# Performance work log

Hardware: AMD Instinct MI355X
Metric: run time of the kernel (lower is better)

The kernel has to match this reference:

```python
import jax, jax.numpy as jnp
import numpy as np

B, LI, LC, H = 16, 2048, 2048, 1024


def setup_inputs() -> dict:
    key = jax.random.key(0)
    k1, k2, k3, k4 = jax.random.split(key, 4)
    inp = jax.random.normal(k1, (B, LI, H), dtype=jnp.float32)
    ctx = jax.random.normal(k2, (B, LC, H), dtype=jnp.float32)
    # mask out the last quarter of context positions (True = masked), never a full row
    context_mask = jnp.broadcast_to(jnp.arange(LC) >= (3 * LC) // 4, (B, LC))
    W = jax.random.normal(k3, (H, H), dtype=jnp.float32) * (1.0 / np.sqrt(H))
    b = jax.random.normal(k4, (H,), dtype=jnp.float32) * 0.01
    return {"input": inp, "context": ctx, "context_mask": context_mask, "W": W, "b": b}


def reference(input, context, context_mask, W, b):
    # shared relu-projected linear for query and key/value sides
    q = jax.nn.relu(jnp.einsum('bih,oh->bio', input, W) + b)    # [B, Li, H]
    k = jax.nn.relu(jnp.einsum('bjh,oh->bjo', context, W) + b)  # [B, Lc, H]
    scores = jnp.einsum('bid,bjd->bij', q, k)                    # [B, Li, Lc], no scaling
    scores = jnp.where(context_mask[:, None, :], -jnp.inf, scores)
    probs = jax.nn.softmax(scores, axis=2)
    return jnp.einsum('bij,bjd->bid', probs, k)                  # weighted sum of context hiddens
```

## Files before the change

kernel.cpp:

```cpp
#include <hip/hip_runtime.h>

typedef _Float16 half8 __attribute__((ext_vector_type(8)));
typedef _Float16 half4 __attribute__((ext_vector_type(4)));
typedef float floatx4 __attribute__((ext_vector_type(4)));

#define OFF_X    0L
#define OFF_S    0L
#define OFF_P    67108864L
#define OFF_W    134217728L
#define OFF_QK   136314880L
#define OFF_KT   270532608L
#define OFF_MASK 337641472L
#define WS_NEED  337674240L

__device__ __forceinline__ void glds16(const void* g, void* l) {
  __builtin_amdgcn_global_load_lds(
      (__attribute__((address_space(1))) void*)(void*)(g),
      (__attribute__((address_space(3))) void*)(l), 16, 0, 0);
}

__global__ void mask_canon(const unsigned* __restrict__ raw,
                           unsigned char* __restrict__ outm) {
  __shared__ int flag;
  int t = threadIdx.x;
  if (t == 0) flag = 0;
  __syncthreads();
  int loc = 0;
  for (int i = t; i < 8192; i += 256)
    if (raw[i] > 1u) loc = 1;
  if (loc) flag = 1;
  __syncthreads();
  if (flag) {
    const unsigned char* b8 = (const unsigned char*)raw;
    for (int j = t; j < 32768; j += 256) outm[j] = (b8[j] != 0);
  } else {
    const int* r32 = (const int*)raw;
    for (int j = t; j < 32768; j += 256) outm[j] = (r32[j] != 0);
  }
}

__global__ __launch_bounds__(256) void cvt_f32_f16(const float* __restrict__ x,
                                                   _Float16* __restrict__ y, long n) {
  long i = ((long)blockIdx.x * 256 + threadIdx.x) * 4;
  if (i + 3 < n) {
    float4 v = *(const float4*)(x + i);
    half4 h;
    h[0] = (_Float16)v.x; h[1] = (_Float16)v.y;
    h[2] = (_Float16)v.z; h[3] = (_Float16)v.w;
    *(half4*)(y + i) = h;
  }
}

template <bool EPI>
__global__ __launch_bounds__(512, 2)
void gemm_nt3(const _Float16* __restrict__ A, long sAz,
              const _Float16* __restrict__ B, long sBz,
              void* __restrict__ Cv, long sCz,
              const float* __restrict__ bias, int K, int ldc) {
  __shared__ _Float16 lds[81920];
  const int t = threadIdx.x;
  const int l = t & 63;
  const int w = t >> 6;
  const int wr = w >> 2, wc = w & 3;
  const int l15 = l & 15, quad = l >> 4;
  const int srow = l >> 3;
  const int gchunk = (l & 7) ^ (srow & 7);
  const int sbase = w * 8;

  const _Float16* Ag = A + (long)blockIdx.z * sAz + (long)blockIdx.y * 256 * (long)K;
  const _Float16* Bg = B + (long)blockIdx.z * sBz + (long)blockIdx.x * 256 * (long)K;

  _Float16* const As = lds;
  _Float16* const Bs = lds + 32768;

  const int arow = wr * 128 + l15;
  const int brow = wc * 64 + l15;
  const int ccA = (quad ^ (arow & 7)) << 3;
  const int ccB = (quad ^ (brow & 7)) << 3;

  floatx4 acc[8][4] = {};
  const int NT = K >> 6;

#define STG(gp, dst, rnd, kt)                                                  \
  glds16(gp + (long)((rnd) * 64 + sbase + srow) * K + (kt) + gchunk * 8,       \
         (dst) + ((rnd) * 64 + sbase) * 64)
#define MM(mh)                                                                 \
  do {                                                                         \
    _Pragma("unroll") for (int mi_ = 0; mi_ < 4; ++mi_)                        \
      _Pragma("unroll") for (int ni_ = 0; ni_ < 4; ++ni_)                      \
        acc[(mh) * 4 + mi_][ni_] = __builtin_amdgcn_mfma_f32_16x16x32_f16(     \
            af[mi_], bf[ni_], acc[(mh) * 4 + mi_][ni_], 0, 0, 0);              \
  } while (0)
#define PH_HEAD()                                                              \
  __builtin_amdgcn_s_barrier();                                                \
  asm volatile("s_waitcnt lgkmcnt(0)" ::: "memory");                           \
  __builtin_amdgcn_s_setprio(1)
#define PH_TAIL()                                                              \
  __builtin_amdgcn_s_setprio(0)

  STG(Ag, As, 0, 0); STG(Ag, As, 1, 0); STG(Ag, As, 2, 0); STG(Ag, As, 3, 0);
  STG(Bg, Bs, 0, 0); STG(Bg, Bs, 1, 0); STG(Bg, Bs, 2, 0); STG(Bg, Bs, 3, 0);
  {
    const int k1 = (NT > 1 ? 64 : 0);
    _Float16* b1 = Bs + 16384;
    STG(Bg, b1, 0, k1); STG(Bg, b1, 1, k1); STG(Bg, b1, 2, k1); STG(Bg, b1, 3, k1);
  }
  asm volatile("s_waitcnt vmcnt(4)" ::: "memory");
  __builtin_amdgcn_s_barrier();

  int bq = 0, bq2 = 2;
  for (int tt = 0; tt < NT; ++tt) {
    const _Float16* Ap = As + (tt & 1) * 16384;
    const _Float16* Bp = Bs + bq * 16384;
    _Float16* Anx = As + ((tt + 1) & 1) * 16384;
    _Float16* Bnx = Bs + bq2 * 16384;
    const int kt1 = ((tt + 1 < NT) ? tt + 1 : NT - 1) << 6;
    const int kt2 = ((tt + 2 < NT) ? tt + 2 : NT - 1) << 6;
    half8 af[4], bf[4];

#pragma unroll
    for (int ni = 0; ni < 4; ++ni) bf[ni] = *(const half8*)(Bp + (brow + ni * 16) * 64 + ccB);
#pragma unroll
    for (int mi = 0; mi < 4; ++mi) af[mi] = *(const half8*)(Ap + (arow + mi * 16) * 64 + ccA);
    STG(Ag, Anx, 0, kt1);
    STG(Ag, Anx, 1, kt1);
    PH_HEAD();
    MM(0);
    PH_TAIL();
    __builtin_amdgcn_s_barrier();

#pragma unroll
    for (int mi = 0; mi < 4; ++mi)
      af[mi] = *(const half8*)(Ap + (arow + (mi + 4) * 16) * 64 + ccA);
    STG(Ag, Anx, 2, kt1);
    STG(Ag, Anx, 3, kt1);
    PH_HEAD();
    MM(1);
    PH_TAIL();
    __builtin_amdgcn_s_barrier();

#pragma unroll
    for (int ni = 0; ni < 4; ++ni)
      bf[ni] = *(const half8*)(Bp + (brow + ni * 16) * 64 + (ccB ^ 32));
#pragma unroll
    for (int mi = 0; mi < 4; ++mi)
      af[mi] = *(const half8*)(Ap + (arow + mi * 16) * 64 + (ccA ^ 32));
    STG(Bg, Bnx, 0, kt2);
    STG(Bg, Bnx, 1, kt2);
    PH_HEAD();
    MM(0);
    PH_TAIL();
    __builtin_amdgcn_s_barrier();

#pragma unroll
    for (int mi = 0; mi < 4; ++mi)
      af[mi] = *(const half8*)(Ap + (arow + (mi + 4) * 16) * 64 + (ccA ^ 32));
    STG(Bg, Bnx, 2, kt2);
    STG(Bg, Bnx, 3, kt2);
    PH_HEAD();
    MM(1);
    PH_TAIL();
    asm volatile("s_waitcnt vmcnt(4)" ::: "memory");
    __builtin_amdgcn_s_barrier();

    bq = (bq == 2) ? 0 : bq + 1;
    bq2 = (bq2 == 2) ? 0 : bq2 + 1;
  }
  asm volatile("s_waitcnt vmcnt(0)" ::: "memory");
  __syncthreads();
#undef STG
#undef MM
#undef PH_HEAD
#undef PH_TAIL

  const long cbase = (long)blockIdx.z * sCz + (long)blockIdx.y * 256 * (long)ldc +
                     (long)blockIdx.x * 256;
  const int rowb = quad * 4;
  if constexpr (EPI) {
    float bv[4];
#pragma unroll
    for (int ni = 0; ni < 4; ++ni) bv[ni] = bias[blockIdx.x * 256 + wc * 64 + ni * 16 + l15];
#pragma unroll
    for (int mi = 0; mi < 8; ++mi)
#pragma unroll
      for (int ni = 0; ni < 4; ++ni) {
        const int col = wc * 64 + ni * 16 + l15;
#pragma unroll
        for (int p = 0; p < 4; ++p) {
          const int row = wr * 128 + mi * 16 + rowb + p;
          lds[row * 264 + (((col >> 3) ^ (row & 7)) << 3) + (col & 7)] =
              (_Float16)fmaxf(acc[mi][ni][p] + bv[ni], 0.f);
        }
      }
    __syncthreads();
    _Float16* Cp = (_Float16*)Cv + cbase;
#pragma unroll
    for (int pp = 0; pp < 16; ++pp) {
      const int r = (t >> 5) + 16 * pp;
      const int c = t & 31;
      half8 v = *(const half8*)(lds + r * 264 + ((c ^ (r & 7)) << 3));
      *(half8*)(Cp + (long)r * ldc + c * 8) = v;
    }
  } else {
    float* Cp = (float*)Cv + cbase;
#pragma unroll
    for (int mi = 0; mi < 8; ++mi)
#pragma unroll
      for (int ni = 0; ni < 4; ++ni) {
        const int col = wc * 64 + ni * 16 + l15;
#pragma unroll
        for (int p = 0; p < 4; ++p) {
          const int row = wr * 128 + mi * 16 + rowb + p;
          Cp[(long)row * ldc + col] = acc[mi][ni][p];
        }
      }
  }
}

__global__ __launch_bounds__(256) void transpose_k(const _Float16* __restrict__ Km,
                                                   _Float16* __restrict__ KT) {
  __shared__ _Float16 tile[64 * 72];
  const int t = threadIdx.x;
  const long b = blockIdx.z;
  const _Float16* src = Km + (b * 2048 + blockIdx.x * 64) * 1024 + blockIdx.y * 64;
  {
    const int jl = t >> 2, hc = (t & 3) * 16;
    half8 v0 = *(const half8*)(src + (long)jl * 1024 + hc);
    half8 v1 = *(const half8*)(src + (long)jl * 1024 + hc + 8);
    *(half8*)&tile[jl * 72 + hc] = v0;
    *(half8*)&tile[jl * 72 + hc + 8] = v1;
  }
  __syncthreads();
  {
    const int hl = t >> 2, jc = (t & 3) * 16;
    half8 o0, o1;
#pragma unroll
    for (int jj = 0; jj < 8; jj++) o0[jj] = tile[(jc + jj) * 72 + hl];
#pragma unroll
    for (int jj = 0; jj < 8; jj++) o1[jj] = tile[(jc + 8 + jj) * 72 + hl];
    long off = (b * 1024 + blockIdx.y * 64 + hl) * 2048 + blockIdx.x * 64 + jc;
    *(half8*)(KT + off) = o0;
    *(half8*)(KT + off + 8) = o1;
  }
}

__global__ __launch_bounds__(256) void softmax_k(const float* __restrict__ S,
                                                 _Float16* __restrict__ P,
                                                 const unsigned char* __restrict__ mask,
                                                 int b0) {
  const int i = blockIdx.x, z = blockIdx.y, t = threadIdx.x;
  const float* s = S + ((long)z * 2048 + i) * 2048;
  const unsigned char* mrow = mask + (long)(b0 + z) * 2048;
  const int base0 = t * 4, base1 = 1024 + t * 4;
  float4 a0 = *(const float4*)(s + base0);
  float4 a1 = *(const float4*)(s + base1);
  float v[8] = {a0.x, a0.y, a0.z, a0.w, a1.x, a1.y, a1.z, a1.w};
  const float NINF = -__builtin_inff();
#pragma unroll
  for (int k = 0; k < 4; k++) {
    if (mrow[base0 + k]) v[k] = NINF;
    if (mrow[base1 + k]) v[4 + k] = NINF;
  }
  float mx = v[0];
#pragma unroll
  for (int k = 1; k < 8; k++) mx = fmaxf(mx, v[k]);
#pragma unroll
  for (int o = 32; o >= 1; o >>= 1) mx = fmaxf(mx, __shfl_xor(mx, o, 64));
  __shared__ float redm[4], reds[4];
  if ((t & 63) == 0) redm[t >> 6] = mx;
  __syncthreads();
  mx = fmaxf(fmaxf(redm[0], redm[1]), fmaxf(redm[2], redm[3]));
  float e[8], sm = 0.f;
#pragma unroll
  for (int k = 0; k < 8; k++) { e[k] = __expf(v[k] - mx); sm += e[k]; }
#pragma unroll
  for (int o = 32; o >= 1; o >>= 1) sm += __shfl_xor(sm, o, 64);
  if ((t & 63) == 0) reds[t >> 6] = sm;
  __syncthreads();
  sm = reds[0] + reds[1] + reds[2] + reds[3];
  const float inv = 1.0f / sm;
  _Float16* p = P + ((long)z * 2048 + i) * 2048;
  half4 h0, h1;
#pragma unroll
  for (int k = 0; k < 4; k++) { h0[k] = (_Float16)(e[k] * inv); h1[k] = (_Float16)(e[4 + k] * inv); }
  *(half4*)(p + base0) = h0;
  *(half4*)(p + base1) = h1;
}

extern "C" void kernel_launch(void* const* d_in, const int* in_sizes, int n_in,
                              void* d_out, int out_size, void* d_ws, size_t ws_size,
                              hipStream_t stream) {
  (void)in_sizes; (void)n_in; (void)out_size;
  if ((long)ws_size < WS_NEED) return;

  const float* inp  = (const float*)d_in[0];
  const float* ctx  = (const float*)d_in[1];
  const unsigned* msk = (const unsigned*)d_in[2];
  const float* W    = (const float*)d_in[3];
  const float* bias = (const float*)d_in[4];
  float* out = (float*)d_out;
  char* ws = (char*)d_ws;

  _Float16* Xf   = (_Float16*)(ws + OFF_X);
  float*    Sb   = (float*)(ws + OFF_S);
  _Float16* Pb   = (_Float16*)(ws + OFF_P);
  _Float16* Wf   = (_Float16*)(ws + OFF_W);
  _Float16* QK   = (_Float16*)(ws + OFF_QK);
  _Float16* KT   = (_Float16*)(ws + OFF_KT);
  unsigned char* Mc = (unsigned char*)(ws + OFF_MASK);

  mask_canon<<<1, 256, 0, stream>>>(msk, Mc);
  cvt_f32_f16<<<32768, 256, 0, stream>>>(inp, Xf, 33554432L);
  cvt_f32_f16<<<32768, 256, 0, stream>>>(ctx, Xf + 33554432L, 33554432L);
  cvt_f32_f16<<<1024, 256, 0, stream>>>(W, Wf, 1048576L);
  gemm_nt3<true><<<dim3(4, 256, 1), 512, 0, stream>>>(Xf, 0L, Wf, 0L, (void*)QK, 0L,
                                                      bias, 1024, 1024);
  transpose_k<<<dim3(32, 16, 16), 256, 0, stream>>>(QK + 32768L * 1024, KT);
  for (int g = 0; g < 2; g++) {
    for (int q = 0; q < 2; q++) {
      const int bp = g * 2 + q;
      const _Float16* Aq = QK + (long)bp * 4 * 2048 * 1024;
      const _Float16* Bk = QK + (32768L + (long)bp * 4 * 2048) * 1024;
      gemm_nt3<false><<<dim3(8, 8, 4), 512, 0, stream>>>(
          Aq, 2048L * 1024, Bk, 2048L * 1024, (void*)Sb, 2048L * 2048, nullptr, 1024, 2048);
      softmax_k<<<dim3(2048, 4), 256, 0, stream>>>(Sb, Pb + (long)q * 4 * 2048 * 2048, Mc, bp * 4);
    }
    gemm_nt3<false><<<dim3(4, 8, 8), 512, 0, stream>>>(
        Pb, 2048L * 2048, KT + (long)g * 8 * 1024 * 2048, 1024L * 2048,
        (void*)(out + (long)g * 8 * 2048 * 1024), 2048L * 1024, nullptr, 2048, 1024);
  }
}
```

Baseline: 852.4 us.

## Double-buffer GEMM register fragments, remap workgroups across XCDs, pad epilogue LDS stride

Restructures the GEMM main loop so that LDS fragment reads for the next MFMA phase are issued into alternate register sets (afP/afQ, bfE/bfO) before the current phase's MFMAs run. Partial lgkmcnt waits replace full drains, so LDS latency can overlap matrix math. It also remaps the linear workgroup index so consecutive tiles are spread across the 8 XCDs, and changes the epilogue LDS row stride from 264 to 268 to alter bank mapping. The extra fragment registers raise VGPR pressure under the 2-wave-per-SIMD launch bound, and the hand-tuned lgkmcnt counts must match the issue order exactly.

```diff
diff --git a/kernel.cpp b/kernel.cpp
--- a/kernel.cpp
+++ b/kernel.cpp
@@ -53,7 +53,7 @@
 
 template <bool EPI>
 __global__ __launch_bounds__(512, 2)
-void gemm_nt3(const _Float16* __restrict__ A, long sAz,
+void gemm_nt5(const _Float16* __restrict__ A, long sAz,
               const _Float16* __restrict__ B, long sBz,
               void* __restrict__ Cv, long sCz,
               const float* __restrict__ bias, int K, int ldc) {
@@ -67,8 +67,20 @@
   const int gchunk = (l & 7) ^ (srow & 7);
   const int sbase = w * 8;
 
-  const _Float16* Ag = A + (long)blockIdx.z * sAz + (long)blockIdx.y * 256 * (long)K;
-  const _Float16* Bg = B + (long)blockIdx.z * sBz + (long)blockIdx.x * 256 * (long)K;
+  unsigned bx, by, bz;
+  {
+    const unsigned gx = gridDim.x, gy = gridDim.y, gz = gridDim.z;
+    const unsigned nwg = gx * gy * gz;
+    unsigned lin = blockIdx.x + gx * (blockIdx.y + gy * blockIdx.z);
+    if ((nwg & 7u) == 0u) lin = (lin & 7u) * (nwg >> 3) + (lin >> 3);
+    bx = lin % gx;
+    const unsigned rem = lin / gx;
+    by = rem % gy;
+    bz = rem / gy;
+  }
+
+  const _Float16* Ag = A + (long)bz * sAz + (long)by * 256 * (long)K;
+  const _Float16* Bg = B + (long)bz * sBz + (long)bx * 256 * (long)K;
 
   _Float16* const As = lds;
   _Float16* const Bs = lds + 32768;
@@ -79,24 +91,32 @@
   const int ccB = (quad ^ (brow & 7)) << 3;
 
   floatx4 acc[8][4] = {};
+  half8 afP[4], afQ[4], bfE[4], bfO[4];
   const int NT = K >> 6;
 
 #define STG(gp, dst, rnd, kt)                                                  \
   glds16(gp + (long)((rnd) * 64 + sbase + srow) * K + (kt) + gchunk * 8,       \
          (dst) + ((rnd) * 64 + sbase) * 64)
-#define MM(mh)                                                                 \
+#define RDA(DST, AP, mh, kx)                                                   \
+  _Pragma("unroll") for (int mi_ = 0; mi_ < 4; ++mi_)                          \
+      DST[mi_] = *(const half8*)((AP) + (arow + ((mh) * 4 + mi_) * 16) * 64 +  \
+                                 (ccA ^ ((kx) * 32)));
+#define RDB(DST, BP, kx)                                                       \
+  _Pragma("unroll") for (int ni_ = 0; ni_ < 4; ++ni_)                          \
+      DST[ni_] = *(const half8*)((BP) + (brow + ni_ * 16) * 64 +               \
+                                 (ccB ^ ((kx) * 32)));
+#define MM(mh, AF, BF)                                                         \
   do {                                                                         \
+    __builtin_amdgcn_s_setprio(1);                                             \
     _Pragma("unroll") for (int mi_ = 0; mi_ < 4; ++mi_)                        \
       _Pragma("unroll") for (int ni_ = 0; ni_ < 4; ++ni_)                      \
         acc[(mh) * 4 + mi_][ni_] = __builtin_amdgcn_mfma_f32_16x16x32_f16(     \
-            af[mi_], bf[ni_], acc[(mh) * 4 + mi_][ni_], 0, 0, 0);              \
+            AF[mi_], BF[ni_], acc[(mh) * 4 + mi_][ni_], 0, 0, 0);              \
+    __builtin_amdgcn_s_setprio(0);                                             \
   } while (0)
-#define PH_HEAD()                                                              \
-  __builtin_amdgcn_s_barrier();                                                \
-  asm volatile("s_waitcnt lgkmcnt(0)" ::: "memory");                           \
-  __builtin_amdgcn_s_setprio(1)
-#define PH_TAIL()                                                              \
-  __builtin_amdgcn_s_setprio(0)
+#define WAIT_LGKM(n)                                                           \
+  asm volatile("s_waitcnt lgkmcnt(" #n ")" ::: "memory");                      \
+  __builtin_amdgcn_sched_barrier(0)
 
   STG(Ag, As, 0, 0); STG(Ag, As, 1, 0); STG(Ag, As, 2, 0); STG(Ag, As, 3, 0);
   STG(Bg, Bs, 0, 0); STG(Bg, Bs, 1, 0); STG(Bg, Bs, 2, 0); STG(Bg, Bs, 3, 0);
@@ -107,79 +127,64 @@
   }
   asm volatile("s_waitcnt vmcnt(4)" ::: "memory");
   __builtin_amdgcn_s_barrier();
+  RDB(bfE, Bs, 0);
+  RDA(afP, As, 0, 0);
 
   int bq = 0, bq2 = 2;
   for (int tt = 0; tt < NT; ++tt) {
-    const _Float16* Ap = As + (tt & 1) * 16384;
-    const _Float16* Bp = Bs + bq * 16384;
+    const _Float16* Ap_ = As + (tt & 1) * 16384;
+    const _Float16* Bp_ = Bs + bq * 16384;
     _Float16* Anx = As + ((tt + 1) & 1) * 16384;
     _Float16* Bnx = Bs + bq2 * 16384;
+    const int bqN = (bq == 2) ? 0 : bq + 1;
+    const _Float16* BpN_ = Bs + bqN * 16384;
     const int kt1 = ((tt + 1 < NT) ? tt + 1 : NT - 1) << 6;
     const int kt2 = ((tt + 2 < NT) ? tt + 2 : NT - 1) << 6;
-    half8 af[4], bf[4];
-
-#pragma unroll
-    for (int ni = 0; ni < 4; ++ni) bf[ni] = *(const half8*)(Bp + (brow + ni * 16) * 64 + ccB);
-#pragma unroll
-    for (int mi = 0; mi < 4; ++mi) af[mi] = *(const half8*)(Ap + (arow + mi * 16) * 64 + ccA);
-    STG(Ag, Anx, 0, kt1);
-    STG(Ag, Anx, 1, kt1);
-    PH_HEAD();
-    MM(0);
-    PH_TAIL();
+
+    RDA(afQ, Ap_, 1, 0);
+    STG(Ag, Anx, 0, kt1); STG(Ag, Anx, 1, kt1);
+    STG(Ag, Anx, 2, kt1); STG(Ag, Anx, 3, kt1);
+    WAIT_LGKM(4);
     __builtin_amdgcn_s_barrier();
-
-#pragma unroll
-    for (int mi = 0; mi < 4; ++mi)
-      af[mi] = *(const half8*)(Ap + (arow + (mi + 4) * 16) * 64 + ccA);
-    STG(Ag, Anx, 2, kt1);
-    STG(Ag, Anx, 3, kt1);
-    PH_HEAD();
-    MM(1);
-    PH_TAIL();
+    MM(0, afP, bfE);
+
+    RDB(bfO, Bp_, 1);
+    RDA(afP, Ap_, 0, 1);
+    STG(Bg, Bnx, 0, kt2); STG(Bg, Bnx, 1, kt2);
+    WAIT_LGKM(8);
     __builtin_amdgcn_s_barrier();
-
-#pragma unroll
-    for (int ni = 0; ni < 4; ++ni)
-      bf[ni] = *(const half8*)(Bp + (brow + ni * 16) * 64 + (ccB ^ 32));
-#pragma unroll
-    for (int mi = 0; mi < 4; ++mi)
-      af[mi] = *(const half8*)(Ap + (arow + mi * 16) * 64 + (ccA ^ 32));
-    STG(Bg, Bnx, 0, kt2);
-    STG(Bg, Bnx, 1, kt2);
-    PH_HEAD();
-    MM(0);
-    PH_TAIL();
+    MM(1, afQ, bfE);
+
+    RDA(afQ, Ap_, 1, 1);
+    STG(Bg, Bnx, 2, kt2); STG(Bg, Bnx, 3, kt2);
+    WAIT_LGKM(4);
     __builtin_amdgcn_s_barrier();
-
-#pragma unroll
-    for (int mi = 0; mi < 4; ++mi)
-      af[mi] = *(const half8*)(Ap + (arow + (mi + 4) * 16) * 64 + (ccA ^ 32));
-    STG(Bg, Bnx, 2, kt2);
-    STG(Bg, Bnx, 3, kt2);
-    PH_HEAD();
-    MM(1);
-    PH_TAIL();
+    MM(0, afP, bfO);
+
     asm volatile("s_waitcnt vmcnt(4)" ::: "memory");
     __builtin_amdgcn_s_barrier();
-
-    bq = (bq == 2) ? 0 : bq + 1;
+    RDB(bfE, BpN_, 0);
+    RDA(afP, Anx, 0, 0);
+    WAIT_LGKM(8);
+    MM(1, afQ, bfO);
+
+    bq = bqN;
     bq2 = (bq2 == 2) ? 0 : bq2 + 1;
   }
   asm volatile("s_waitcnt vmcnt(0)" ::: "memory");
   __syncthreads();
 #undef STG
+#undef RDA
+#undef RDB
 #undef MM
-#undef PH_HEAD
-#undef PH_TAIL
-
-  const long cbase = (long)blockIdx.z * sCz + (long)blockIdx.y * 256 * (long)ldc +
-                     (long)blockIdx.x * 256;
+#undef WAIT_LGKM
+
+  const long cbase = (long)bz * sCz + (long)by * 256 * (long)ldc + (long)bx * 256;
   const int rowb = quad * 4;
   if constexpr (EPI) {
     float bv[4];
 #pragma unroll
-    for (int ni = 0; ni < 4; ++ni) bv[ni] = bias[blockIdx.x * 256 + wc * 64 + ni * 16 + l15];
+    for (int ni = 0; ni < 4; ++ni) bv[ni] = bias[bx * 256 + wc * 64 + ni * 16 + l15];
 #pragma unroll
     for (int mi = 0; mi < 8; ++mi)
 #pragma unroll
@@ -188,7 +193,7 @@
 #pragma unroll
         for (int p = 0; p < 4; ++p) {
           const int row = wr * 128 + mi * 16 + rowb + p;
-          lds[row * 264 + (((col >> 3) ^ (row & 7)) << 3) + (col & 7)] =
+          lds[row * 268 + (((col >> 3) ^ (row & 7)) << 3) + (col & 7)] =
               (_Float16)fmaxf(acc[mi][ni][p] + bv[ni], 0.f);
         }
       }
@@ -198,7 +203,7 @@
     for (int pp = 0; pp < 16; ++pp) {
       const int r = (t >> 5) + 16 * pp;
       const int c = t & 31;
-      half8 v = *(const half8*)(lds + r * 264 + ((c ^ (r & 7)) << 3));
+      half8 v = *(const half8*)(lds + r * 268 + ((c ^ (r & 7)) << 3));
       *(half8*)(Cp + (long)r * ldc + c * 8) = v;
     }
   } else {
@@ -313,7 +318,7 @@
   cvt_f32_f16<<<32768, 256, 0, stream>>>(inp, Xf, 33554432L);
   cvt_f32_f16<<<32768, 256, 0, stream>>>(ctx, Xf + 33554432L, 33554432L);
   cvt_f32_f16<<<1024, 256, 0, stream>>>(W, Wf, 1048576L);
-  gemm_nt3<true><<<dim3(4, 256, 1), 512, 0, stream>>>(Xf, 0L, Wf, 0L, (void*)QK, 0L,
+  gemm_nt5<true><<<dim3(4, 256, 1), 512, 0, stream>>>(Xf, 0L, Wf, 0L, (void*)QK, 0L,
                                                       bias, 1024, 1024);
   transpose_k<<<dim3(32, 16, 16), 256, 0, stream>>>(QK + 32768L * 1024, KT);
   for (int g = 0; g < 2; g++) {
@@ -321,11 +326,11 @@
       const int bp = g * 2 + q;
       const _Float16* Aq = QK + (long)bp * 4 * 2048 * 1024;
       const _Float16* Bk = QK + (32768L + (long)bp * 4 * 2048) * 1024;
-      gemm_nt3<false><<<dim3(8, 8, 4), 512, 0, stream>>>(
+      gemm_nt5<false><<<dim3(8, 8, 4), 512, 0, stream>>>(
           Aq, 2048L * 1024, Bk, 2048L * 1024, (void*)Sb, 2048L * 2048, nullptr, 1024, 2048);
       softmax_k<<<dim3(2048, 4), 256, 0, stream>>>(Sb, Pb + (long)q * 4 * 2048 * 2048, Mc, bp * 4);
     }
-    gemm_nt3<false><<<dim3(4, 8, 8), 512, 0, stream>>>(
+    gemm_nt5<false><<<dim3(4, 8, 8), 512, 0, stream>>>(
         Pb, 2048L * 2048, KT + (long)g * 8 * 1024 * 2048, 1024L * 2048,
         (void*)(out + (long)g * 8 * 2048 * 1024), 2048L * 1024, nullptr, 2048, 1024);
   }
```

Result: no change. 836.1 us (-1.9%).
